# Kernel tuning notes

Measured on AMD Instinct MI355X. Metric: run time of the kernel, lower is better.

Reference implementation:

```python
import jax, jax.numpy as jnp
import numpy as np

# Grid constants (from init_kwargs)
N_PIX_LO = 256
OVERSAMP = 4
N_PIX_HI = N_PIX_LO * OVERSAMP          # 1024
PIXSCALE_LO = 0.1                        # arcsec / low-res pixel
PIXSCALE_HI = PIXSCALE_LO / OVERSAMP     # arcsec / hi-res pixel
FOV_HALF_HI = 0.5 * (N_PIX_HI - 1) * PIXSCALE_HI
NV = 64
VEL0 = 0.0
DV = 10.0
M = 4_000_000                            # total cloudlet samples (N_clouds * K_vel)

# 8 trilinear corner offsets (x fastest pattern matches torch stacks)
OX = jnp.array([0, 0, 0, 0, 1, 1, 1, 1], dtype=jnp.int32)
OY = jnp.array([0, 0, 1, 1, 0, 0, 1, 1], dtype=jnp.int32)
OV = jnp.array([0, 1, 0, 1, 0, 1, 0, 1], dtype=jnp.int32)


def setup_inputs() -> dict:
    key = jax.random.key(0)
    k1, k2, k3, k4 = jax.random.split(key, 4)
    # positions mostly inside the FoV so most points survive the in-bounds mask
    ra = (jax.random.uniform(k1, (M,), dtype=jnp.float32) - 0.5) * (2.0 * FOV_HALF_HI * 0.95)
    dec = (jax.random.uniform(k2, (M,), dtype=jnp.float32) - 0.5) * (2.0 * FOV_HALF_HI * 0.95)
    vel = jax.random.uniform(k3, (M,), dtype=jnp.float32) * (DV * (NV - 2))
    flux = jax.random.uniform(k4, (M,), dtype=jnp.float32)
    return {"ra": ra, "dec": dec, "vel": vel, "flux": flux}


def _index_and_frac(x):
    i0 = jnp.floor(x)
    return i0.astype(jnp.int32), x - i0


def reference(ra, dec, vel, flux):
    # continuous hi-res grid coordinates
    ix0, fx = _index_and_frac((ra + FOV_HALF_HI) / PIXSCALE_HI)
    iy0, fy = _index_and_frac((dec + FOV_HALF_HI) / PIXSCALE_HI)
    iv0, fv = _index_and_frac((vel - VEL0) / DV)

    # in-bounds mask (instead of boolean compaction, for static shapes under jit)
    mask = ((ix0 >= 0) & (ix0 < N_PIX_HI - 1)
            & (iy0 >= 0) & (iy0 < N_PIX_HI - 1)
            & (iv0 >= 0) & (iv0 < NV - 1))

    # [M, 8] corner indices
    ix = ix0[:, None] + OX
    iy = iy0[:, None] + OY
    iv = iv0[:, None] + OV

    # [M, 8] trilinear weights: (1-f) for offset 0, f for offset 1
    wx = jnp.where(OX == 0, 1.0 - fx[:, None], fx[:, None])
    wy = jnp.where(OY == 0, 1.0 - fy[:, None], fy[:, None])
    wv = jnp.where(OV == 0, 1.0 - fv[:, None], fv[:, None])

    f_w = flux[:, None] * (wx * wy * wv) * mask[:, None].astype(flux.dtype)

    idx = (iv * N_PIX_HI + iy) * N_PIX_HI + ix          # flat voxel index [M, 8]
    idx = jnp.where(mask[:, None], idx, 0)              # out-of-bounds -> bin 0, weight 0

    cube_flat = jnp.zeros(NV * N_PIX_HI * N_PIX_HI, dtype=flux.dtype)
    cube_flat = cube_flat.at[idx.reshape(-1)].add(f_w.reshape(-1))

    # box-downsample: (Nv, H_lo, s, W_lo, s) -> mean over the two oversample axes
    cube_hi = cube_flat.reshape(NV, N_PIX_LO, OVERSAMP, N_PIX_LO, OVERSAMP)
    cube_lo = cube_hi.mean(axis=(-1, -3))               # (Nv, N_pix_lo, N_pix_lo)
    return cube_lo
```

## Files before the change

kernel.cpp:

```cpp
#include <hip/hip_runtime.h>
#include <hip/hip_fp16.h>

constexpr int   kNpixHi = 1024;
constexpr int   kNpixLo = 256;
constexpr int   kNv     = 64;
constexpr float kFov    = 12.7875f;
constexpr float kPsHi   = 0.025f;
constexpr float kDv     = 10.0f;
constexpr float kVel0   = 0.0f;

constexpr int kTileW        = 128;
constexpr int kTileH        = 64;
constexpr int kBinsPerPlane = 8;
constexpr int kNumBins      = 64 * kBinsPerPlane;
constexpr int kBinCapIdeal  = 16384;
constexpr int kBinCapMin    = 13500;
constexpr int kThreadsK1    = 512;
constexpr int kWavesK1      = kThreadsK1 / 64;
constexpr int kSamplesPerBlock = 4096;
constexpr int kLdsRecCap    = 8192;
constexpr int kThreadsK2    = 1024;

typedef unsigned int u32x4 __attribute__((ext_vector_type(4)));
typedef unsigned long long u64;

__device__ __forceinline__ u64 pack_rec(unsigned idx, float w0, float w1) {
  const unsigned pk = (unsigned)__half_as_ushort(__float2half(w0))
                    | ((unsigned)__half_as_ushort(__float2half(w1)) << 16);
  return ((u64)pk << 16) | idx;
}

__device__ __forceinline__ void sys_store64(u64* p, u64 v) {
  __hip_atomic_store(p, v, __ATOMIC_RELAXED, __HIP_MEMORY_SCOPE_SYSTEM);
}

__device__ __forceinline__ __half2 h2_from_u32(unsigned pk) {
  return __builtin_bit_cast(__half2, pk);
}

enum EmitMode { kCount, kLds, kDirect };

template <EmitMode MODE>
__device__ __forceinline__ void emit(int bin, unsigned idx, float w0, float w1,
                                     unsigned int* s_cnt,
                                     const unsigned int* s_base,
                                     const unsigned int* s_ofs,
                                     u64* lds_rec,
                                     u64* __restrict__ recs,
                                     unsigned int binCap) {
  if (MODE == kCount) {
    atomicAdd(&s_cnt[bin], 1u);
    return;
  }
  const unsigned off = atomicAdd(&s_cnt[bin], 1u);
  if (MODE == kLds) {
    lds_rec[s_ofs[bin] + off] = pack_rec(idx, w0, w1);
  } else {
    const unsigned slot = s_base[bin] + off;
    if (slot < binCap)
      sys_store64(&recs[(size_t)bin * binCap + slot], pack_rec(idx, w0, w1));
  }
}

template <EmitMode MODE>
__device__ __forceinline__ void process_sample(float rr, float dd, float vv, float ff,
                                               unsigned int* s_cnt,
                                               const unsigned int* s_base,
                                               const unsigned int* s_ofs,
                                               u64* lds_rec,
                                               u64* __restrict__ recs,
                                               unsigned int binCap) {
  const float x = (rr + kFov) / kPsHi;
  const float y = (dd + kFov) / kPsHi;
  const float w = (vv - kVel0) / kDv;

  const float xf = floorf(x), yf = floorf(y), wf = floorf(w);
  const int ix0 = (int)xf, iy0 = (int)yf, iv0 = (int)wf;

  if (ix0 < 0 || ix0 >= kNpixHi - 1 ||
      iy0 < 0 || iy0 >= kNpixHi - 1 ||
      iv0 < 0 || iv0 >= kNv - 1)
    return;

  const float fx = x - xf, fy = y - yf, fv = w - wf;

  const float fw  = ff * 0.0625f;
  const float wv0 = fw * (1.0f - fv);
  const float wv1 = fw * fv;

  const int lx0 = ix0 >> 2, lx1 = (ix0 + 1) >> 2;
  const int ly0 = iy0 >> 2, ly1 = (iy0 + 1) >> 2;
  const bool tx = (lx1 != lx0), ty = (ly1 != ly0);
  const float wx0 = tx ? (1.0f - fx) : 1.0f;
  const float wy0 = ty ? (1.0f - fy) : 1.0f;

#define EMIT_PIX(lx, ly, wxy)                                                \
  {                                                                          \
    const int sb  = (((ly) >> 6) << 1) | ((lx) >> 7);                        \
    const int bin = (iv0 << 3) | sb;                                         \
    const unsigned idx = (unsigned)(((ly) & (kTileH - 1)) * kTileW +         \
                                    ((lx) & (kTileW - 1)));                  \
    emit<MODE>(bin, idx, (wxy) * wv0, (wxy) * wv1,                           \
               s_cnt, s_base, s_ofs, lds_rec, recs, binCap);                 \
  }

  EMIT_PIX(lx0, ly0, wx0 * wy0)
  if (tx)       EMIT_PIX(lx1, ly0, fx * wy0)
  if (ty)       EMIT_PIX(lx0, ly1, wx0 * fy)
  if (tx && ty) EMIT_PIX(lx1, ly1, fx * fy)
#undef EMIT_PIX
}

__global__ __launch_bounds__(kThreadsK1) void scatter_kernel(
    const float* __restrict__ ra, const float* __restrict__ dec,
    const float* __restrict__ vel, const float* __restrict__ flux,
    u64* __restrict__ recs, unsigned int* __restrict__ cursors,
    int m, unsigned int binCap) {
  __shared__ unsigned int s_cnt[kNumBins];
  __shared__ unsigned int s_base[kNumBins];
  __shared__ unsigned int s_ofs[kNumBins];
  __shared__ unsigned int s_wbase[kWavesK1];
  __shared__ unsigned int s_wsum[kWavesK1];
  __shared__ unsigned int s_total;
  __shared__ u64 lds_rec[kLdsRecCap];

  const int tid = threadIdx.x;
  const int blockBase = blockIdx.x * kSamplesPerBlock;
  const int sA = blockBase + tid * 4;
  const int sB = blockBase + kThreadsK1 * 4 + tid * 4;

  float4 rA, dA, vA, fA, rB, dB, vB, fB;

#define LOAD4(s0, r4, d4, v4, f4)                                          \
  if ((s0) + 4 <= m) {                                                     \
    r4 = *reinterpret_cast<const float4*>(ra + (s0));                      \
    d4 = *reinterpret_cast<const float4*>(dec + (s0));                     \
    v4 = *reinterpret_cast<const float4*>(vel + (s0));                     \
    f4 = *reinterpret_cast<const float4*>(flux + (s0));                    \
  } else {                                                                 \
    float* rp = &r4.x; float* dp = &d4.x; float* vp = &v4.x; float* fp = &f4.x; \
    _Pragma("unroll")                                                      \
    for (int k = 0; k < 4; ++k) {                                          \
      const int i = (s0) + k;                                              \
      const bool in = (i < m);                                             \
      rp[k] = in ? ra[i]   : 0.0f;                                         \
      dp[k] = in ? dec[i]  : 0.0f;                                         \
      vp[k] = in ? vel[i]  : -1e9f;                                        \
      fp[k] = in ? flux[i] : 0.0f;                                         \
    }                                                                      \
  }

  LOAD4(sA, rA, dA, vA, fA)
  LOAD4(sB, rB, dB, vB, fB)
#undef LOAD4

  s_cnt[tid] = 0u;
  __syncthreads();

#pragma unroll
  for (int k = 0; k < 4; ++k)
    process_sample<kCount>((&rA.x)[k], (&dA.x)[k], (&vA.x)[k], (&fA.x)[k],
                           s_cnt, s_base, s_ofs, lds_rec, recs, binCap);
#pragma unroll
  for (int k = 0; k < 4; ++k)
    process_sample<kCount>((&rB.x)[k], (&dB.x)[k], (&vB.x)[k], (&fB.x)[k],
                           s_cnt, s_base, s_ofs, lds_rec, recs, binCap);
  __syncthreads();

  const unsigned c = s_cnt[tid];
  unsigned v = c;
#pragma unroll
  for (int d = 1; d < 64; d <<= 1) {
    const unsigned n = __shfl_up(v, d, 64);
    if ((tid & 63) >= d) v += n;
  }
  if ((tid & 63) == 63) s_wsum[tid >> 6] = v;
  __syncthreads();
  if (tid == 0) {
    unsigned acc = 0;
#pragma unroll
    for (int i = 0; i < kWavesK1; ++i) { s_wbase[i] = acc; acc += s_wsum[i]; }
    s_total = acc;
  }
  __syncthreads();
  s_ofs[tid]  = s_wbase[tid >> 6] + v - c;
  s_base[tid] = c ? atomicAdd(&cursors[tid], c) : 0u;
  s_cnt[tid]  = 0u;
  __syncthreads();

  const bool ldsPath = (s_total <= (unsigned)kLdsRecCap);

  if (ldsPath) {
#pragma unroll
    for (int k = 0; k < 4; ++k)
      process_sample<kLds>((&rA.x)[k], (&dA.x)[k], (&vA.x)[k], (&fA.x)[k],
                           s_cnt, s_base, s_ofs, lds_rec, recs, binCap);
#pragma unroll
    for (int k = 0; k < 4; ++k)
      process_sample<kLds>((&rB.x)[k], (&dB.x)[k], (&vB.x)[k], (&fB.x)[k],
                           s_cnt, s_base, s_ofs, lds_rec, recs, binCap);
    __syncthreads();

    const int wave = tid >> 6, lane = tid & 63;
    for (int b = wave; b < kNumBins; b += kWavesK1) {
      const unsigned cnt  = s_cnt[b];
      const unsigned ofs  = s_ofs[b];
      const unsigned base = s_base[b];
      u64* __restrict__ seg = recs + (size_t)b * binCap;
      for (unsigned j = lane; j < cnt; j += 64) {
        const unsigned slot = base + j;
        if (slot < binCap) sys_store64(&seg[slot], lds_rec[ofs + j]);
      }
    }
  } else {
#pragma unroll
    for (int k = 0; k < 4; ++k)
      process_sample<kDirect>((&rA.x)[k], (&dA.x)[k], (&vA.x)[k], (&fA.x)[k],
                              s_cnt, s_base, s_ofs, lds_rec, recs, binCap);
#pragma unroll
    for (int k = 0; k < 4; ++k)
      process_sample<kDirect>((&rB.x)[k], (&dB.x)[k], (&vB.x)[k], (&fB.x)[k],
                              s_cnt, s_base, s_ofs, lds_rec, recs, binCap);
  }
}

__device__ __forceinline__ void accum_bin(__half2* tile2,
                                          const u64* __restrict__ rb,
                                          unsigned cnt, int tid) {
  const u32x4* __restrict__ rb4 = reinterpret_cast<const u32x4*>(rb);
  const unsigned npair = cnt >> 1;
  for (unsigned j = (unsigned)tid; j < npair; j += kThreadsK2) {
    const u32x4 q = rb4[j];
    const unsigned idx0 = q.x & 0xFFFFu;
    const unsigned pk0  = (q.x >> 16) | (q.y << 16);
    unsafeAtomicAdd(&tile2[idx0], h2_from_u32(pk0));
    const unsigned idx1 = q.z & 0xFFFFu;
    const unsigned pk1  = (q.z >> 16) | (q.w << 16);
    unsafeAtomicAdd(&tile2[idx1], h2_from_u32(pk1));
  }
  if ((cnt & 1u) && tid == 0) {
    const u64 r = rb[cnt - 1];
    const unsigned idx = (unsigned)r & 0xFFFFu;
    const unsigned pk  = (unsigned)(r >> 16);
    unsafeAtomicAdd(&tile2[idx], h2_from_u32(pk));
  }
}

__global__ __launch_bounds__(kThreadsK2) void accum_even(
    const u64* __restrict__ recs, const unsigned int* __restrict__ cursors,
    float* __restrict__ out, unsigned int binCap) {
  __shared__ __half2 tile2[kTileH * kTileW];
  const int b   = blockIdx.x;
  const int tid = threadIdx.x;
  const int iv  = 2 * (b >> 3);
  const int sb  = b & 7;
  const int bin = (iv << 3) | sb;

  for (int i = tid; i < kTileH * kTileW; i += kThreadsK2)
    reinterpret_cast<unsigned*>(tile2)[i] = 0u;
  __syncthreads();

  unsigned cnt = cursors[bin];
  if (cnt > binCap) cnt = binCap;
  accum_bin(tile2, recs + (size_t)bin * binCap, cnt, tid);
  __syncthreads();

  const int t_y = sb >> 1, t_x = sb & 1;
  const size_t spBase = (size_t)(t_y * kTileH) * kNpixLo + t_x * kTileW;
  const size_t baseA = (size_t)iv * (kNpixLo * kNpixLo) + spBase;
  const size_t baseB = baseA + kNpixLo * kNpixLo;
  for (int g = tid; g < (kTileH * kTileW) / 4; g += kThreadsK2) {
    const int pix = g * 4;
    const int ry = pix >> 7, rx = pix & (kTileW - 1);
    float4 a, bv;
#pragma unroll
    for (int k = 0; k < 4; ++k) {
      const float2 f = __half22float2(tile2[pix + k]);
      (&a.x)[k] = f.x; (&bv.x)[k] = f.y;
    }
    *reinterpret_cast<float4*>(&out[baseA + (size_t)ry * kNpixLo + rx]) = a;
    *reinterpret_cast<float4*>(&out[baseB + (size_t)ry * kNpixLo + rx]) = bv;
  }
}

__global__ __launch_bounds__(kThreadsK2) void accum_odd(
    const u64* __restrict__ recs, const unsigned int* __restrict__ cursors,
    float* __restrict__ out, unsigned int binCap) {
  __shared__ __half2 tile2[kTileH * kTileW];
  const int b   = blockIdx.x;
  const int tid = threadIdx.x;
  const int iv  = 2 * (b >> 3) + 1;
  const int sb  = b & 7;
  const int bin = (iv << 3) | sb;

  for (int i = tid; i < kTileH * kTileW; i += kThreadsK2)
    reinterpret_cast<unsigned*>(tile2)[i] = 0u;
  __syncthreads();

  unsigned cnt = cursors[bin];
  if (cnt > binCap) cnt = binCap;
  accum_bin(tile2, recs + (size_t)bin * binCap, cnt, tid);
  __syncthreads();

  const int t_y = sb >> 1, t_x = sb & 1;
  const size_t spBase = (size_t)(t_y * kTileH) * kNpixLo + t_x * kTileW;
  const size_t baseA = (size_t)iv * (kNpixLo * kNpixLo) + spBase;
  const size_t baseB = baseA + kNpixLo * kNpixLo;
  for (int g = tid; g < (kTileH * kTileW) / 4; g += kThreadsK2) {
    const int pix = g * 4;
    const int ry = pix >> 7, rx = pix & (kTileW - 1);
    float4 a = *reinterpret_cast<float4*>(&out[baseA + (size_t)ry * kNpixLo + rx]);
    float4 bv = *reinterpret_cast<float4*>(&out[baseB + (size_t)ry * kNpixLo + rx]);
#pragma unroll
    for (int k = 0; k < 4; ++k) {
      const float2 f = __half22float2(tile2[pix + k]);
      (&a.x)[k] += f.x; (&bv.x)[k] += f.y;
    }
    *reinterpret_cast<float4*>(&out[baseA + (size_t)ry * kNpixLo + rx]) = a;
    *reinterpret_cast<float4*>(&out[baseB + (size_t)ry * kNpixLo + rx]) = bv;
  }
}

__device__ __forceinline__ void splat2(float* __restrict__ out, int planeBase,
                                       int lx, int ly, float wxy,
                                       float wv0, float wv1) {
  const int s = ly * kNpixLo + lx;
  unsafeAtomicAdd(out + planeBase + s, wxy * wv0);
  unsafeAtomicAdd(out + planeBase + kNpixLo * kNpixLo + s, wxy * wv1);
}

__global__ __launch_bounds__(256) void cloud_raster_direct(
    const float* __restrict__ ra, const float* __restrict__ dec,
    const float* __restrict__ vel, const float* __restrict__ flux,
    float* __restrict__ out, int m) {
  const int t    = blockIdx.x * blockDim.x + threadIdx.x;
  const int base = t * 4;
  if (base >= m) return;
  float4 r4, d4, v4, f4;
  if (base + 4 <= m) {
    r4 = *reinterpret_cast<const float4*>(ra + base);
    d4 = *reinterpret_cast<const float4*>(dec + base);
    v4 = *reinterpret_cast<const float4*>(vel + base);
    f4 = *reinterpret_cast<const float4*>(flux + base);
  } else {
    float* rp = &r4.x; float* dp = &d4.x; float* vp = &v4.x; float* fp = &f4.x;
#pragma unroll
    for (int k = 0; k < 4; ++k) {
      const int i = base + k;
      rp[k] = (i < m) ? ra[i]   : 0.0f;
      dp[k] = (i < m) ? dec[i]  : 0.0f;
      vp[k] = (i < m) ? vel[i]  : -1e9f;
      fp[k] = (i < m) ? flux[i] : 0.0f;
    }
  }
#pragma unroll
  for (int k = 0; k < 4; ++k) {
    const float rr = (&r4.x)[k], dd = (&d4.x)[k], vv = (&v4.x)[k], ff = (&f4.x)[k];
    const float x = (rr + kFov) / kPsHi;
    const float y = (dd + kFov) / kPsHi;
    const float w = (vv - kVel0) / kDv;
    const float xf = floorf(x), yf = floorf(y), wf = floorf(w);
    const int ix0 = (int)xf, iy0 = (int)yf, iv0 = (int)wf;
    if (ix0 < 0 || ix0 >= kNpixHi - 1 || iy0 < 0 || iy0 >= kNpixHi - 1 ||
        iv0 < 0 || iv0 >= kNv - 1)
      continue;
    const float fx = x - xf, fy = y - yf, fv = w - wf;
    const float fw  = ff * 0.0625f;
    const float wv0 = fw * (1.0f - fv);
    const float wv1 = fw * fv;
    const int lx0 = ix0 >> 2, lx1 = (ix0 + 1) >> 2;
    const int ly0 = iy0 >> 2, ly1 = (iy0 + 1) >> 2;
    const bool tx = (lx1 != lx0), ty = (ly1 != ly0);
    const float wx0 = tx ? (1.0f - fx) : 1.0f;
    const float wy0 = ty ? (1.0f - fy) : 1.0f;
    const int pb = iv0 * (kNpixLo * kNpixLo);
    splat2(out, pb, lx0, ly0, wx0 * wy0, wv0, wv1);
    if (tx)       splat2(out, pb, lx1, ly0, fx  * wy0, wv0, wv1);
    if (ty)       splat2(out, pb, lx0, ly1, wx0 * fy,  wv0, wv1);
    if (tx && ty) splat2(out, pb, lx1, ly1, fx  * fy,  wv0, wv1);
  }
}


extern "C" void kernel_launch(void* const* d_in, const int* in_sizes, int n_in,
                              void* d_out, int out_size, void* d_ws, size_t ws_size,
                              hipStream_t stream) {
  (void)n_in;
  const float* ra   = (const float*)d_in[0];
  const float* dec  = (const float*)d_in[1];
  const float* vel  = (const float*)d_in[2];
  const float* flux = (const float*)d_in[3];
  float* out = (float*)d_out;
  const int m = in_sizes[0];

  constexpr size_t kCursorBytes = 4096;
  unsigned int binCap = 0;
  if (ws_size > kCursorBytes) {
    const size_t avail = (ws_size - kCursorBytes) / ((size_t)kNumBins * 8);
    binCap = (unsigned int)(avail < (size_t)kBinCapIdeal ? avail : (size_t)kBinCapIdeal);
    binCap &= ~1u;
  }

  if (binCap >= kBinCapMin) {
    unsigned int* cursors = (unsigned int*)d_ws;
    u64* recs = (u64*)((char*)d_ws + kCursorBytes);
    hipError_t e = hipMemsetAsync(d_ws, 0, kCursorBytes, stream); (void)e;
    const int blocks = (m + kSamplesPerBlock - 1) / kSamplesPerBlock;
    scatter_kernel<<<blocks, kThreadsK1, 0, stream>>>(ra, dec, vel, flux, recs, cursors, m, binCap);
    accum_even<<<256, kThreadsK2, 0, stream>>>(recs, cursors, out, binCap);
    accum_odd<<<248, kThreadsK2, 0, stream>>>(recs, cursors, out, binCap);
  } else {
    hipError_t e = hipMemsetAsync(d_out, 0, (size_t)out_size * sizeof(float), stream); (void)e;
    const int threads = 256;
    const int nThreads = (m + 3) / 4;
    const int blocks = (nThreads + threads - 1) / threads;
    cloud_raster_direct<<<blocks, threads, 0, stream>>>(ra, dec, vel, flux, out, m);
  }
}
```

Before: 109.0 us.

## Merge even/odd accumulation into one launch plus separate plane-combine kernel

The two dependent accumulate launches (even planes, then odd planes doing read-modify-write on the output) are replaced by one launch over all 512 bins that writes packed half2 tiles to workspace. A new conversion kernel then forms each output plane by adding a bin's low half to the previous plane's high half. This removes the serialization between the even and odd passes and lets all bins run concurrently. In exchange it needs an extra 16 MB round trip through workspace and one more launch. The fallback path also switches from unsafe to safe float atomics.

```diff
diff --git a/kernel.cpp b/kernel.cpp
--- a/kernel.cpp
+++ b/kernel.cpp
@@ -11,6 +11,7 @@
 
 constexpr int kTileW        = 128;
 constexpr int kTileH        = 64;
+constexpr int kTilePix      = kTileW * kTileH;
 constexpr int kBinsPerPlane = 8;
 constexpr int kNumBins      = 64 * kBinsPerPlane;
 constexpr int kBinCapIdeal  = 16384;
@@ -224,10 +225,22 @@
   }
 }
 
-__device__ __forceinline__ void accum_bin(__half2* tile2,
-                                          const u64* __restrict__ rb,
-                                          unsigned cnt, int tid) {
+__global__ __launch_bounds__(kThreadsK2) void accum_kernel(
+    const u64* __restrict__ recs, const unsigned int* __restrict__ cursors,
+    unsigned int* __restrict__ tiles, unsigned int binCap) {
+  __shared__ __half2 tile2[kTilePix];
+  const int bin = blockIdx.x;
+  const int tid = threadIdx.x;
+
+  for (int i = tid; i < kTilePix; i += kThreadsK2)
+    reinterpret_cast<unsigned*>(tile2)[i] = 0u;
+  __syncthreads();
+
+  unsigned cnt = cursors[bin];
+  if (cnt > binCap) cnt = binCap;
+  const u64* __restrict__ rb = recs + (size_t)bin * binCap;
   const u32x4* __restrict__ rb4 = reinterpret_cast<const u32x4*>(rb);
+
   const unsigned npair = cnt >> 1;
   for (unsigned j = (unsigned)tid; j < npair; j += kThreadsK2) {
     const u32x4 q = rb4[j];
@@ -240,93 +253,56 @@
   }
   if ((cnt & 1u) && tid == 0) {
     const u64 r = rb[cnt - 1];
-    const unsigned idx = (unsigned)r & 0xFFFFu;
-    const unsigned pk  = (unsigned)(r >> 16);
-    unsafeAtomicAdd(&tile2[idx], h2_from_u32(pk));
-  }
-}
-
-__global__ __launch_bounds__(kThreadsK2) void accum_even(
-    const u64* __restrict__ recs, const unsigned int* __restrict__ cursors,
-    float* __restrict__ out, unsigned int binCap) {
-  __shared__ __half2 tile2[kTileH * kTileW];
-  const int b   = blockIdx.x;
-  const int tid = threadIdx.x;
-  const int iv  = 2 * (b >> 3);
-  const int sb  = b & 7;
-  const int bin = (iv << 3) | sb;
-
-  for (int i = tid; i < kTileH * kTileW; i += kThreadsK2)
-    reinterpret_cast<unsigned*>(tile2)[i] = 0u;
-  __syncthreads();
-
-  unsigned cnt = cursors[bin];
-  if (cnt > binCap) cnt = binCap;
-  accum_bin(tile2, recs + (size_t)bin * binCap, cnt, tid);
-  __syncthreads();
-
-  const int t_y = sb >> 1, t_x = sb & 1;
-  const size_t spBase = (size_t)(t_y * kTileH) * kNpixLo + t_x * kTileW;
-  const size_t baseA = (size_t)iv * (kNpixLo * kNpixLo) + spBase;
-  const size_t baseB = baseA + kNpixLo * kNpixLo;
-  for (int g = tid; g < (kTileH * kTileW) / 4; g += kThreadsK2) {
-    const int pix = g * 4;
-    const int ry = pix >> 7, rx = pix & (kTileW - 1);
-    float4 a, bv;
-#pragma unroll
-    for (int k = 0; k < 4; ++k) {
-      const float2 f = __half22float2(tile2[pix + k]);
-      (&a.x)[k] = f.x; (&bv.x)[k] = f.y;
-    }
-    *reinterpret_cast<float4*>(&out[baseA + (size_t)ry * kNpixLo + rx]) = a;
-    *reinterpret_cast<float4*>(&out[baseB + (size_t)ry * kNpixLo + rx]) = bv;
-  }
-}
-
-__global__ __launch_bounds__(kThreadsK2) void accum_odd(
-    const u64* __restrict__ recs, const unsigned int* __restrict__ cursors,
-    float* __restrict__ out, unsigned int binCap) {
-  __shared__ __half2 tile2[kTileH * kTileW];
-  const int b   = blockIdx.x;
-  const int tid = threadIdx.x;
-  const int iv  = 2 * (b >> 3) + 1;
-  const int sb  = b & 7;
-  const int bin = (iv << 3) | sb;
-
-  for (int i = tid; i < kTileH * kTileW; i += kThreadsK2)
-    reinterpret_cast<unsigned*>(tile2)[i] = 0u;
-  __syncthreads();
-
-  unsigned cnt = cursors[bin];
-  if (cnt > binCap) cnt = binCap;
-  accum_bin(tile2, recs + (size_t)bin * binCap, cnt, tid);
-  __syncthreads();
-
-  const int t_y = sb >> 1, t_x = sb & 1;
-  const size_t spBase = (size_t)(t_y * kTileH) * kNpixLo + t_x * kTileW;
-  const size_t baseA = (size_t)iv * (kNpixLo * kNpixLo) + spBase;
-  const size_t baseB = baseA + kNpixLo * kNpixLo;
-  for (int g = tid; g < (kTileH * kTileW) / 4; g += kThreadsK2) {
-    const int pix = g * 4;
-    const int ry = pix >> 7, rx = pix & (kTileW - 1);
-    float4 a = *reinterpret_cast<float4*>(&out[baseA + (size_t)ry * kNpixLo + rx]);
-    float4 bv = *reinterpret_cast<float4*>(&out[baseB + (size_t)ry * kNpixLo + rx]);
-#pragma unroll
-    for (int k = 0; k < 4; ++k) {
-      const float2 f = __half22float2(tile2[pix + k]);
-      (&a.x)[k] += f.x; (&bv.x)[k] += f.y;
-    }
-    *reinterpret_cast<float4*>(&out[baseA + (size_t)ry * kNpixLo + rx]) = a;
-    *reinterpret_cast<float4*>(&out[baseB + (size_t)ry * kNpixLo + rx]) = bv;
-  }
+    unsafeAtomicAdd(&tile2[(unsigned)r & 0xFFFFu],
+                    h2_from_u32((unsigned)(r >> 16)));
+  }
+  __syncthreads();
+
+  unsigned int* __restrict__ dst = tiles + (size_t)bin * kTilePix;
+  const unsigned* __restrict__ src = reinterpret_cast<const unsigned*>(tile2);
+  for (int g = tid; g < kTilePix / 4; g += kThreadsK2) {
+    *reinterpret_cast<u32x4*>(dst + g * 4) =
+        *reinterpret_cast<const u32x4*>(src + g * 4);
+  }
+}
+
+__global__ __launch_bounds__(256) void convert_kernel(
+    const unsigned int* __restrict__ tiles, float* __restrict__ out) {
+  const int t   = blockIdx.x * blockDim.x + threadIdx.x;
+  const int bin = t >> 11;
+  const int g   = t & 2047;
+  const int idx = g * 4;
+
+  const u32x4 cur = *reinterpret_cast<const u32x4*>(
+      tiles + (size_t)bin * kTilePix + idx);
+  const int v = bin >> 3;
+  u32x4 prv = {0u, 0u, 0u, 0u};
+  if (v > 0)
+    prv = *reinterpret_cast<const u32x4*>(
+        tiles + (size_t)(bin - kBinsPerPlane) * kTilePix + idx);
+
+  float4 r;
+#pragma unroll
+  for (int k = 0; k < 4; ++k) {
+    const __half2 c = h2_from_u32(cur[k]);
+    const __half2 p = h2_from_u32(prv[k]);
+    (&r.x)[k] = __low2float(c) + ((v > 0) ? __high2float(p) : 0.0f);
+  }
+
+  const int sb = bin & 7;
+  const int ry = idx >> 7, rx = idx & (kTileW - 1);
+  const size_t o = (size_t)v * (kNpixLo * kNpixLo)
+                 + (size_t)((sb >> 1) * kTileH + ry) * kNpixLo
+                 + (size_t)(sb & 1) * kTileW + rx;
+  *reinterpret_cast<float4*>(out + o) = r;
 }
 
 __device__ __forceinline__ void splat2(float* __restrict__ out, int planeBase,
                                        int lx, int ly, float wxy,
                                        float wv0, float wv1) {
   const int s = ly * kNpixLo + lx;
-  unsafeAtomicAdd(out + planeBase + s, wxy * wv0);
-  unsafeAtomicAdd(out + planeBase + kNpixLo * kNpixLo + s, wxy * wv1);
+  atomicAdd(out + planeBase + s, wxy * wv0);
+  atomicAdd(out + planeBase + kNpixLo * kNpixLo + s, wxy * wv1);
 }
 
 __global__ __launch_bounds__(256) void cloud_raster_direct(
@@ -394,21 +370,23 @@
   const int m = in_sizes[0];
 
   constexpr size_t kCursorBytes = 4096;
+  constexpr size_t kTileBytes   = (size_t)kNumBins * kTilePix * 4;
   unsigned int binCap = 0;
-  if (ws_size > kCursorBytes) {
-    const size_t avail = (ws_size - kCursorBytes) / ((size_t)kNumBins * 8);
+  if (ws_size > kCursorBytes + kTileBytes) {
+    const size_t avail = (ws_size - kCursorBytes - kTileBytes) / ((size_t)kNumBins * 8);
     binCap = (unsigned int)(avail < (size_t)kBinCapIdeal ? avail : (size_t)kBinCapIdeal);
     binCap &= ~1u;
   }
 
   if (binCap >= kBinCapMin) {
     unsigned int* cursors = (unsigned int*)d_ws;
-    u64* recs = (u64*)((char*)d_ws + kCursorBytes);
+    unsigned int* tiles   = (unsigned int*)((char*)d_ws + kCursorBytes);
+    u64* recs = (u64*)((char*)d_ws + kCursorBytes + kTileBytes);
     hipError_t e = hipMemsetAsync(d_ws, 0, kCursorBytes, stream); (void)e;
     const int blocks = (m + kSamplesPerBlock - 1) / kSamplesPerBlock;
     scatter_kernel<<<blocks, kThreadsK1, 0, stream>>>(ra, dec, vel, flux, recs, cursors, m, binCap);
-    accum_even<<<256, kThreadsK2, 0, stream>>>(recs, cursors, out, binCap);
-    accum_odd<<<248, kThreadsK2, 0, stream>>>(recs, cursors, out, binCap);
+    accum_kernel<<<kNumBins, kThreadsK2, 0, stream>>>(recs, cursors, tiles, binCap);
+    convert_kernel<<<(kNumBins * (kTilePix / 4)) / 256, 256, 0, stream>>>(tiles, out);
   } else {
     hipError_t e = hipMemsetAsync(d_out, 0, (size_t)out_size * sizeof(float), stream); (void)e;
     const int threads = 256;
```

Measured after the change: 107.7 us. About the same (-1.2%).
